# Optimization experiments

Hardware: AMD Instinct MI355X
Metric: run time of the kernel (lower is better)

Reference implementation:

```python
import jax, jax.numpy as jnp
import numpy as np

N, H, V = 4096, 1024, 16384


def setup_inputs() -> dict:
    key = jax.random.key(0)
    k1, k2, k3, k4 = jax.random.split(key, 4)
    _input = jax.random.normal(k1, (N, H), dtype=jnp.float32)
    weight = jax.random.normal(k2, (V, H), dtype=jnp.float32) * (1.0 / np.sqrt(H))
    target = jax.random.normal(k3, (N, V), dtype=jnp.float32)
    bias = jax.random.normal(k4, (V,), dtype=jnp.float32)
    return {"_input": _input, "weight": weight, "target": target, "bias": bias}


def reference(_input, weight, target, bias):
    # Fused linear + MSE with reduction='mean':
    # logits = _input @ weight.T + bias  -> (N, V)
    # loss = mean((logits - target)**2) over all N*V elements
    logits = jnp.einsum("nh,vh->nv", _input, weight) + bias
    diff = logits - target
    return jnp.mean(diff * diff)
```

## Files before the change

### kernel.cpp

```cpp
#include <hip/hip_runtime.h>
#include <hip/hip_bf16.h>
#include <stdint.h>

#define N_ 4096
#define H_ 1024
#define V_ 16384

using i32x8  = __attribute__((ext_vector_type(8))) int;
using f32x16 = __attribute__((ext_vector_type(16))) float;

__global__ void cast_f32_to_fp8(const float* __restrict__ in, uint8_t* __restrict__ out) {
    size_t i = ((size_t)blockIdx.x * blockDim.x + threadIdx.x) * 8;
    float4 a = *(const float4*)(in + i);
    float4 b = *(const float4*)(in + i + 4);
    int lo = __builtin_amdgcn_cvt_pk_fp8_f32(a.x, a.y, 0, 0);
    lo     = __builtin_amdgcn_cvt_pk_fp8_f32(a.z, a.w, lo, 1);
    int hi = __builtin_amdgcn_cvt_pk_fp8_f32(b.x, b.y, 0, 0);
    hi     = __builtin_amdgcn_cvt_pk_fp8_f32(b.z, b.w, hi, 1);
    *(int2*)(out + i) = make_int2(lo, hi);
}

#define BM 128
#define BN 128
#define BK 64

__global__ __launch_bounds__(256, 2) void gemm_mse(
    const uint8_t* __restrict__ A8,
    const uint8_t* __restrict__ W8,
    const float*  __restrict__ target,
    const float*  __restrict__ bias,
    float* __restrict__ partials)
{
    __shared__ uint8_t As[8 * 1024];
    __shared__ uint8_t Bs[8 * 1024];
    __shared__ float red[4];

    const int tid  = threadIdx.x;
    const int w    = tid >> 6;
    const int lane = tid & 63;
    const int l32  = lane & 31;
    const int half = lane >> 5;
    const int wm   = w >> 1;
    const int wn   = w & 1;

    const int rowBase = blockIdx.y * BM;
    const int colBase = blockIdx.x * BN;

    f32x16 acc[2][2];
#pragma unroll
    for (int i = 0; i < 2; ++i)
#pragma unroll
        for (int j = 0; j < 2; ++j)
#pragma unroll
            for (int r = 0; r < 16; ++r) acc[i][j][r] = 0.f;

    const int ldrow = lane >> 2;
    const int ldkq  = (lane & 3) ^ ((ldrow + (ldrow >> 2)) & 3);

    const int rl  = lane & 15;
    const int rcb = (lane >> 4) & 1;
    const int fl  = (rl + (rl >> 2)) & 3;
    const uint8_t* aPtr[2][2];
    const uint8_t* bPtr[2][2];
#pragma unroll
    for (int i = 0; i < 2; ++i)
#pragma unroll
        for (int c = 0; c < 2; ++c) {
            const int slot = rl * 4 + (((half << 1) + c) ^ fl);
            aPtr[i][c] = As + (size_t)((wm * 2 + i) * 2 + rcb) * 1024 + slot * 16;
            bPtr[i][c] = Bs + (size_t)((wn * 2 + i) * 2 + rcb) * 1024 + slot * 16;
        }

    for (int k0 = 0; k0 < H_; k0 += BK) {
        __syncthreads();
#pragma unroll
        for (int c = 0; c < 2; ++c) {
            const int chunkid = w * 2 + c;
            const uint8_t* ga = A8 + (size_t)(rowBase + chunkid * 16 + ldrow) * H_ + k0 + ldkq * 16;
            __builtin_amdgcn_global_load_lds(
                (const __attribute__((address_space(1))) void*)ga,
                (__attribute__((address_space(3))) void*)(As + chunkid * 1024), 16, 0, 0);
            const uint8_t* gb = W8 + (size_t)(colBase + chunkid * 16 + ldrow) * H_ + k0 + ldkq * 16;
            __builtin_amdgcn_global_load_lds(
                (const __attribute__((address_space(1))) void*)gb,
                (__attribute__((address_space(3))) void*)(Bs + chunkid * 1024), 16, 0, 0);
        }
        __syncthreads();

        i32x8 af[2], bq[2];
#pragma unroll
        for (int i = 0; i < 2; ++i) {
            int4 a0 = *(const int4*)aPtr[i][0];
            int4 a1 = *(const int4*)aPtr[i][1];
            af[i][0] = a0.x; af[i][1] = a0.y; af[i][2] = a0.z; af[i][3] = a0.w;
            af[i][4] = a1.x; af[i][5] = a1.y; af[i][6] = a1.z; af[i][7] = a1.w;
            int4 b0 = *(const int4*)bPtr[i][0];
            int4 b1 = *(const int4*)bPtr[i][1];
            bq[i][0] = b0.x; bq[i][1] = b0.y; bq[i][2] = b0.z; bq[i][3] = b0.w;
            bq[i][4] = b1.x; bq[i][5] = b1.y; bq[i][6] = b1.z; bq[i][7] = b1.w;
        }
#pragma unroll
        for (int i = 0; i < 2; ++i)
#pragma unroll
            for (int j = 0; j < 2; ++j)
                acc[i][j] = __builtin_amdgcn_mfma_scale_f32_32x32x64_f8f6f4(
                    af[i], bq[j], acc[i][j],
                    0 , 0 ,
                    0, 0x7F7F7F7F,
                    0, 0x7F7F7F7F);
    }

    float sum = 0.f;
    float biasj[2];
#pragma unroll
    for (int j = 0; j < 2; ++j) biasj[j] = bias[colBase + wn * 64 + j * 32 + l32];

#pragma unroll
    for (int i = 0; i < 2; ++i) {
#pragma unroll
        for (int r = 0; r < 16; ++r) {
            const int row = (r & 3) + 8 * (r >> 2) + 4 * half;
            const int gm = rowBase + wm * 64 + i * 32 + row;
            const float* trow = target + (size_t)gm * V_ + colBase + wn * 64 + l32;
#pragma unroll
            for (int j = 0; j < 2; ++j) {
                float d = acc[i][j][r] + biasj[j] - trow[j * 32];
                sum += d * d;
            }
        }
    }

#pragma unroll
    for (int off = 32; off; off >>= 1) sum += __shfl_down(sum, off, 64);
    if (lane == 0) red[w] = sum;
    __syncthreads();
    if (tid == 0)
        partials[blockIdx.y * gridDim.x + blockIdx.x] = red[0] + red[1] + red[2] + red[3];
}

__global__ void finalize_kernel(const float* __restrict__ partials, float* __restrict__ out, int n) {
    float s = 0.f;
    for (int i = threadIdx.x; i < n; i += 256) s += partials[i];
#pragma unroll
    for (int off = 32; off; off >>= 1) s += __shfl_down(s, off, 64);
    __shared__ float red[4];
    const int w = threadIdx.x >> 6, lane = threadIdx.x & 63;
    if (lane == 0) red[w] = s;
    __syncthreads();
    if (threadIdx.x == 0)
        out[0] = (red[0] + red[1] + red[2] + red[3]) * (1.0f / ((float)N_ * (float)V_));
}

extern "C" void kernel_launch(void* const* d_in, const int* in_sizes, int n_in,
                              void* d_out, int out_size, void* d_ws, size_t ws_size,
                              hipStream_t stream) {
    const float* input  = (const float*)d_in[0];
    const float* weight = (const float*)d_in[1];
    const float* target = (const float*)d_in[2];
    const float* bias   = (const float*)d_in[3];
    float* out = (float*)d_out;

    uint8_t* A8 = (uint8_t*)d_ws;
    uint8_t* W8 = A8 + (size_t)N_ * H_;
    float* partials = (float*)(W8 + (size_t)V_ * H_);

    cast_f32_to_fp8<<<(N_ * H_) / (256 * 8), 256, 0, stream>>>(input, A8);
    cast_f32_to_fp8<<<(V_ * H_) / (256 * 8), 256, 0, stream>>>(weight, W8);

    dim3 grid(V_ / BN, N_ / BM);
    gemm_mse<<<grid, 256, 0, stream>>>(A8, W8, target, bias, partials);

    finalize_kernel<<<1, 256, 0, stream>>>(partials, out, (V_ / BN) * (N_ / BM));
}
```

Measured before the change: 457.9 us.

## Double K-tile depth, remap blocks per XCD, and merge the two cast kernels

The GEMM now stages two 64-wide K slices per iteration (BK=128), which halves the number of barrier pairs per K loop at the cost of twice the LDS per block. Blocks are launched as a flat grid and remapped so each XCD (flat & 7) gets a contiguous strip of 16 column tiles, meant to improve L2 reuse of weight tiles. The two fp8 cast launches are merged into one kernel to save a launch. The larger LDS footprint (32KB per block) may lower occupancy alongside launch_bounds(256,2).

```diff
diff --git a/kernel.cpp b/kernel.cpp
--- a/kernel.cpp
+++ b/kernel.cpp
@@ -9,8 +9,15 @@
 using i32x8  = __attribute__((ext_vector_type(8))) int;
 using f32x16 = __attribute__((ext_vector_type(16))) float;
 
-__global__ void cast_f32_to_fp8(const float* __restrict__ in, uint8_t* __restrict__ out) {
-    size_t i = ((size_t)blockIdx.x * blockDim.x + threadIdx.x) * 8;
+__global__ void cast2_f32_to_fp8(const float* __restrict__ in0, uint8_t* __restrict__ out0,
+                                 const float* __restrict__ in1, uint8_t* __restrict__ out1,
+                                 int nblk0) {
+    const float* in;
+    uint8_t* out;
+    int bid;
+    if (blockIdx.x < (unsigned)nblk0) { in = in0; out = out0; bid = blockIdx.x; }
+    else                              { in = in1; out = out1; bid = blockIdx.x - nblk0; }
+    size_t i = ((size_t)bid * blockDim.x + threadIdx.x) * 8;
     float4 a = *(const float4*)(in + i);
     float4 b = *(const float4*)(in + i + 4);
     int lo = __builtin_amdgcn_cvt_pk_fp8_f32(a.x, a.y, 0, 0);
@@ -22,7 +29,7 @@
 
 #define BM 128
 #define BN 128
-#define BK 64
+#define BK 128
 
 __global__ __launch_bounds__(256, 2) void gemm_mse(
     const uint8_t* __restrict__ A8,
@@ -31,8 +38,8 @@
     const float*  __restrict__ bias,
     float* __restrict__ partials)
 {
-    __shared__ uint8_t As[8 * 1024];
-    __shared__ uint8_t Bs[8 * 1024];
+    __shared__ uint8_t As[2 * 8 * 1024];
+    __shared__ uint8_t Bs[2 * 8 * 1024];
     __shared__ float red[4];
 
     const int tid  = threadIdx.x;
@@ -43,8 +50,14 @@
     const int wm   = w >> 1;
     const int wn   = w & 1;
 
-    const int rowBase = blockIdx.y * BM;
-    const int colBase = blockIdx.x * BN;
+    const int flat = blockIdx.x;
+    const int xcd  = flat & 7;
+    const int idx  = flat >> 3;
+    const int tx   = xcd * 16 + (idx & 15);
+    const int ty   = idx >> 4;
+
+    const int rowBase = ty * BM;
+    const int colBase = tx * BN;
 
     f32x16 acc[2][2];
 #pragma unroll
@@ -74,40 +87,47 @@
     for (int k0 = 0; k0 < H_; k0 += BK) {
         __syncthreads();
 #pragma unroll
-        for (int c = 0; c < 2; ++c) {
-            const int chunkid = w * 2 + c;
-            const uint8_t* ga = A8 + (size_t)(rowBase + chunkid * 16 + ldrow) * H_ + k0 + ldkq * 16;
-            __builtin_amdgcn_global_load_lds(
-                (const __attribute__((address_space(1))) void*)ga,
-                (__attribute__((address_space(3))) void*)(As + chunkid * 1024), 16, 0, 0);
-            const uint8_t* gb = W8 + (size_t)(colBase + chunkid * 16 + ldrow) * H_ + k0 + ldkq * 16;
-            __builtin_amdgcn_global_load_lds(
-                (const __attribute__((address_space(1))) void*)gb,
-                (__attribute__((address_space(3))) void*)(Bs + chunkid * 1024), 16, 0, 0);
+        for (int h = 0; h < 2; ++h) {
+#pragma unroll
+            for (int c = 0; c < 2; ++c) {
+                const int chunkid = w * 2 + c;
+                const int kOff = k0 + h * 64 + ldkq * 16;
+                const uint8_t* ga = A8 + (size_t)(rowBase + chunkid * 16 + ldrow) * H_ + kOff;
+                __builtin_amdgcn_global_load_lds(
+                    (const __attribute__((address_space(1))) void*)ga,
+                    (__attribute__((address_space(3))) void*)(As + h * 8192 + chunkid * 1024), 16, 0, 0);
+                const uint8_t* gb = W8 + (size_t)(colBase + chunkid * 16 + ldrow) * H_ + kOff;
+                __builtin_amdgcn_global_load_lds(
+                    (const __attribute__((address_space(1))) void*)gb,
+                    (__attribute__((address_space(3))) void*)(Bs + h * 8192 + chunkid * 1024), 16, 0, 0);
+            }
         }
         __syncthreads();
 
-        i32x8 af[2], bq[2];
 #pragma unroll
-        for (int i = 0; i < 2; ++i) {
-            int4 a0 = *(const int4*)aPtr[i][0];
-            int4 a1 = *(const int4*)aPtr[i][1];
-            af[i][0] = a0.x; af[i][1] = a0.y; af[i][2] = a0.z; af[i][3] = a0.w;
-            af[i][4] = a1.x; af[i][5] = a1.y; af[i][6] = a1.z; af[i][7] = a1.w;
-            int4 b0 = *(const int4*)bPtr[i][0];
-            int4 b1 = *(const int4*)bPtr[i][1];
-            bq[i][0] = b0.x; bq[i][1] = b0.y; bq[i][2] = b0.z; bq[i][3] = b0.w;
-            bq[i][4] = b1.x; bq[i][5] = b1.y; bq[i][6] = b1.z; bq[i][7] = b1.w;
+        for (int h = 0; h < 2; ++h) {
+            i32x8 af[2], bq[2];
+#pragma unroll
+            for (int i = 0; i < 2; ++i) {
+                int4 a0 = *(const int4*)(aPtr[i][0] + h * 8192);
+                int4 a1 = *(const int4*)(aPtr[i][1] + h * 8192);
+                af[i][0] = a0.x; af[i][1] = a0.y; af[i][2] = a0.z; af[i][3] = a0.w;
+                af[i][4] = a1.x; af[i][5] = a1.y; af[i][6] = a1.z; af[i][7] = a1.w;
+                int4 b0 = *(const int4*)(bPtr[i][0] + h * 8192);
+                int4 b1 = *(const int4*)(bPtr[i][1] + h * 8192);
+                bq[i][0] = b0.x; bq[i][1] = b0.y; bq[i][2] = b0.z; bq[i][3] = b0.w;
+                bq[i][4] = b1.x; bq[i][5] = b1.y; bq[i][6] = b1.z; bq[i][7] = b1.w;
+            }
+#pragma unroll
+            for (int i = 0; i < 2; ++i)
+#pragma unroll
+                for (int j = 0; j < 2; ++j)
+                    acc[i][j] = __builtin_amdgcn_mfma_scale_f32_32x32x64_f8f6f4(
+                        af[i], bq[j], acc[i][j],
+                        0 , 0 ,
+                        0, 0x7F7F7F7F,
+                        0, 0x7F7F7F7F);
         }
-#pragma unroll
-        for (int i = 0; i < 2; ++i)
-#pragma unroll
-            for (int j = 0; j < 2; ++j)
-                acc[i][j] = __builtin_amdgcn_mfma_scale_f32_32x32x64_f8f6f4(
-                    af[i], bq[j], acc[i][j],
-                    0 , 0 ,
-                    0, 0x7F7F7F7F,
-                    0, 0x7F7F7F7F);
     }
 
     float sum = 0.f;
@@ -135,7 +155,7 @@
     if (lane == 0) red[w] = sum;
     __syncthreads();
     if (tid == 0)
-        partials[blockIdx.y * gridDim.x + blockIdx.x] = red[0] + red[1] + red[2] + red[3];
+        partials[flat] = red[0] + red[1] + red[2] + red[3];
 }
 
 __global__ void finalize_kernel(const float* __restrict__ partials, float* __restrict__ out, int n) {
@@ -164,11 +184,12 @@
     uint8_t* W8 = A8 + (size_t)N_ * H_;
     float* partials = (float*)(W8 + (size_t)V_ * H_);
 
-    cast_f32_to_fp8<<<(N_ * H_) / (256 * 8), 256, 0, stream>>>(input, A8);
-    cast_f32_to_fp8<<<(V_ * H_) / (256 * 8), 256, 0, stream>>>(weight, W8);
+    const int nblk0 = (N_ * H_) / (256 * 8);
+    const int nblk1 = (V_ * H_) / (256 * 8);
+    cast2_f32_to_fp8<<<nblk0 + nblk1, 256, 0, stream>>>(input, A8, weight, W8, nblk0);
 
-    dim3 grid(V_ / BN, N_ / BM);
-    gemm_mse<<<grid, 256, 0, stream>>>(A8, W8, target, bias, partials);
+    const int nblocks = (V_ / BN) * (N_ / BM);
+    gemm_mse<<<nblocks, 256, 0, stream>>>(A8, W8, target, bias, partials);
 
-    finalize_kernel<<<1, 256, 0, stream>>>(partials, out, (V_ / BN) * (N_ / BM));
+    finalize_kernel<<<1, 256, 0, stream>>>(partials, out, nblocks);
 }
```

New measurement: 451.2 us. No clear change (-1.5%).
